# Performance work log

Measured on AMD Instinct MI355X. Metric: run time of the kernel, lower is better.

Reference implementation:

```python
import jax, jax.numpy as jnp
import numpy as np

B, T, D, H = 2, 2048, 1024, 16
HD = D // H  # head dim = 64

def build_rope(t, half, base=10000.0):
    inv = 1.0 / (base ** (jnp.arange(0, half, dtype=jnp.float32) / half))
    ang = jnp.arange(t, dtype=jnp.float32)[:, None] * inv[None, :]  # (T, half)
    return jnp.stack([jnp.cos(ang), jnp.sin(ang)], axis=-1)  # (T, half, 2)

def setup_inputs() -> dict:
    key = jax.random.key(0)
    k1, k2, k3 = jax.random.split(key, 3)
    x = jax.random.normal(k1, (B, T, D), dtype=jnp.float32)
    W_attn = jax.random.normal(k2, (D, 3 * D), dtype=jnp.float32) * (1.0 / np.sqrt(D))
    W_proj = jax.random.normal(k3, (D, D), dtype=jnp.float32) * (1.0 / np.sqrt(D))
    rope = build_rope(T, HD // 2)
    mask = jnp.tril(jnp.ones((T, T), dtype=bool))[None, None]  # (1,1,T,T) causal
    return {"x": x, "rope": rope, "W_attn": W_attn, "W_proj": W_proj, "mask": mask}

def apply_rope(xq, rope):
    # xq: (B, T, H, HD); rope: (T, HD//2, 2)
    xs = xq.astype(jnp.float32).reshape(*xq.shape[:-1], -1, 2)        # (B,T,H,HD/2,2)
    rc = rope[:xq.shape[1]].reshape(1, xq.shape[1], 1, xs.shape[3], 2)  # (1,T,1,HD/2,2)
    out = jnp.stack([
        xs[..., 0] * rc[..., 0] - xs[..., 1] * rc[..., 1],
        xs[..., 1] * rc[..., 0] + xs[..., 0] * rc[..., 1],
    ], axis=-1)
    return out.reshape(xq.shape).astype(xq.dtype)

def reference(x, rope, W_attn, W_proj, mask):
    b, t, d = x.shape
    qkv = x @ W_attn                                   # (B,T,3D)
    q, k, v = jnp.split(qkv, 3, axis=2)
    q = apply_rope(q.reshape(b, t, H, HD), rope)
    k = apply_rope(k.reshape(b, t, H, HD), rope)
    v = v.reshape(b, t, H, HD)
    # (B,H,T,HD)
    q = q.transpose(0, 2, 1, 3)
    k = k.transpose(0, 2, 1, 3)
    v = v.transpose(0, 2, 1, 3)
    scale = 1.0 / np.sqrt(HD)
    scores = jnp.einsum('bhqd,bhkd->bhqk', q, k) * scale
    scores = jnp.where(mask, scores, jnp.finfo(scores.dtype).min)
    attn = jax.nn.softmax(scores, axis=-1)
    out = jnp.einsum('bhqk,bhkd->bhqd', attn, v)       # (B,H,T,HD)
    out = out.transpose(0, 2, 1, 3).reshape(b, t, d)
    return out @ W_proj
```

## Files before the change

kernel.cpp:

```cpp
#include <hip/hip_runtime.h>


typedef __bf16 bf16x8 __attribute__((ext_vector_type(8)));
typedef float f32x4 __attribute__((ext_vector_type(4)));

__device__ __forceinline__ float bf2f(unsigned short u) {
  unsigned int i = ((unsigned int)u) << 16;
  return __builtin_bit_cast(float, i);
}
__device__ __forceinline__ unsigned short f2bf(float f) {
  unsigned int i = __builtin_bit_cast(unsigned int, f);
  i += 0x7FFFu + ((i >> 16) & 1u);
  return (unsigned short)(i >> 16);
}

__device__ __forceinline__ void gload_lds16(const unsigned short* g, unsigned short* l) {
  __builtin_amdgcn_global_load_lds(
      (const __attribute__((address_space(1))) void*)g,
      (__attribute__((address_space(3))) void*)l, 16, 0, 0);
}

__global__ __launch_bounds__(256) void convert_f32_bf16_kernel(
    const float* __restrict__ in, unsigned short* __restrict__ outp, int n8)
{
  int i = blockIdx.x * 256 + threadIdx.x;
  if (i >= n8) return;
  const float4 a0 = *reinterpret_cast<const float4*>(&in[(size_t)i * 8]);
  const float4 a1 = *reinterpret_cast<const float4*>(&in[(size_t)i * 8 + 4]);
  uint4 pk;
  pk.x = (unsigned int)f2bf(a0.x) | ((unsigned int)f2bf(a0.y) << 16);
  pk.y = (unsigned int)f2bf(a0.z) | ((unsigned int)f2bf(a0.w) << 16);
  pk.z = (unsigned int)f2bf(a1.x) | ((unsigned int)f2bf(a1.y) << 16);
  pk.w = (unsigned int)f2bf(a1.z) | ((unsigned int)f2bf(a1.w) << 16);
  *reinterpret_cast<uint4*>(&outp[(size_t)i * 8]) = pk;
}

__global__ __launch_bounds__(256) void convert_transpose_kernel(
    const float* __restrict__ W, unsigned short* __restrict__ WT, int R, int C)
{
  __shared__ unsigned short tileT[64][72];
  const int c0 = blockIdx.x * 64, r0 = blockIdx.y * 64;
  const int tid = threadIdx.x;
  const int rr = tid >> 4, cc = (tid & 15) * 4;
#pragma unroll
  for (int it = 0; it < 4; ++it) {
    int gr = r0 + rr + it * 16;
    float4 v = *reinterpret_cast<const float4*>(&W[(size_t)gr * C + c0 + cc]);
    tileT[cc + 0][rr + it * 16] = f2bf(v.x);
    tileT[cc + 1][rr + it * 16] = f2bf(v.y);
    tileT[cc + 2][rr + it * 16] = f2bf(v.z);
    tileT[cc + 3][rr + it * 16] = f2bf(v.w);
  }
  __syncthreads();
  const int wc = tid >> 2, wk = (tid & 3) * 16;
  uint4 o0 = *reinterpret_cast<const uint4*>(&tileT[wc][wk]);
  uint4 o1 = *reinterpret_cast<const uint4*>(&tileT[wc][wk + 8]);
  unsigned short* dst = &WT[(size_t)(c0 + wc) * R + r0 + wk];
  *reinterpret_cast<uint4*>(dst) = o0;
  *reinterpret_cast<uint4*>(dst + 8) = o1;
}

__global__ __launch_bounds__(256) void transpose_v_kernel(
    const unsigned short* __restrict__ Vb, unsigned short* __restrict__ VT)
{
  __shared__ unsigned short tl[64][72];
  const int bh = blockIdx.y;
  const int t0 = blockIdx.x * 64;
  const int tid = threadIdx.x;
  const unsigned short* src = Vb + (size_t)bh * 2048 * 64;
  unsigned short* dst = VT + (size_t)bh * 64 * 2048;
  int row = tid >> 3, c8 = (tid & 7) * 8;
#pragma unroll
  for (int it = 0; it < 2; ++it, row += 32) {
    uint4 v = *reinterpret_cast<const uint4*>(&src[(size_t)(t0 + row) * 64 + c8]);
    *reinterpret_cast<uint4*>(&tl[row][c8]) = v;
  }
  __syncthreads();
  const int d = tid >> 2, tc = (tid & 3) * 16;
  unsigned int o[8];
#pragma unroll
  for (int j = 0; j < 8; ++j) {
    unsigned int lo  = tl[tc + 2 * j][d];
    unsigned int hi2 = tl[tc + 2 * j + 1][d];
    o[j] = lo | (hi2 << 16);
  }
  unsigned short* dp = &dst[(size_t)d * 2048 + t0 + tc];
  *reinterpret_cast<uint4*>(dp)     = uint4{o[0], o[1], o[2], o[3]};
  *reinterpret_cast<uint4*>(dp + 8) = uint4{o[4], o[5], o[6], o[7]};
}

template<bool C_IS_F32>
__global__ __launch_bounds__(256) void gemm_bt_kernel(
    const unsigned short* __restrict__ A, const unsigned short* __restrict__ BT,
    void* __restrict__ Cp, int M, int N, int K)
{
  __shared__ alignas(16) unsigned short As[128 * 32];
  __shared__ alignas(16) unsigned short Bs[128 * 32];

  const int tid = threadIdx.x;
  const int m0 = blockIdx.y * 128, n0 = blockIdx.x * 128;
  const int w = tid >> 6, lane = tid & 63;
  const int wr = (w >> 1) * 64, wc = (w & 1) * 64;
  const int g = lane >> 4, r = lane & 15;

  f32x4 acc[4][4];
#pragma unroll
  for (int i = 0; i < 4; ++i)
#pragma unroll
    for (int j = 0; j < 4; ++j)
      acc[i][j] = f32x4{0.f, 0.f, 0.f, 0.f};

  const int srow = w * 32 + (lane >> 2);
  const int sk = (lane & 3) << 3;
  const size_t a_base = (size_t)(m0 + srow) * K + sk;
  const size_t b_base = (size_t)(n0 + srow) * K + sk;
  unsigned short* lA = &As[w * 1024 + lane * 8];
  unsigned short* lB = &Bs[w * 1024 + lane * 8];
  const size_t rstep = (size_t)16 * K;

  for (int k0 = 0; k0 < K; k0 += 32) {
    __syncthreads();
    gload_lds16(&A[a_base + k0], lA);
    gload_lds16(&A[a_base + k0 + rstep], lA + 512);
    gload_lds16(&BT[b_base + k0], lB);
    gload_lds16(&BT[b_base + k0 + rstep], lB + 512);
    __syncthreads();

    bf16x8 af[4], bff[4];
#pragma unroll
    for (int i = 0; i < 4; ++i)
      af[i] = __builtin_bit_cast(bf16x8,
          *reinterpret_cast<const uint4*>(&As[(wr + i * 16 + r) * 32 + g * 8]));
#pragma unroll
    for (int j = 0; j < 4; ++j)
      bff[j] = __builtin_bit_cast(bf16x8,
          *reinterpret_cast<const uint4*>(&Bs[(wc + j * 16 + r) * 32 + g * 8]));
#pragma unroll
    for (int i = 0; i < 4; ++i)
#pragma unroll
      for (int j = 0; j < 4; ++j)
        acc[i][j] = __builtin_amdgcn_mfma_f32_16x16x32_bf16(af[i], bff[j], acc[i][j], 0, 0, 0);
  }

#pragma unroll
  for (int i = 0; i < 4; ++i)
#pragma unroll
    for (int j = 0; j < 4; ++j)
#pragma unroll
      for (int reg = 0; reg < 4; ++reg) {
        int row = m0 + wr + i * 16 + g * 4 + reg;
        int col = n0 + wc + j * 16 + r;
        if constexpr (C_IS_F32)
          ((float*)Cp)[(size_t)row * N + col] = acc[i][j][reg];
        else
          ((unsigned short*)Cp)[(size_t)row * N + col] = f2bf(acc[i][j][reg]);
      }
}

__global__ __launch_bounds__(256) void rope_scatter_kernel(
    const unsigned short* __restrict__ qkv, const float* __restrict__ rope,
    unsigned short* __restrict__ Qb, unsigned short* __restrict__ Kb,
    unsigned short* __restrict__ Vb)
{
  int gid = blockIdx.x * 256 + threadIdx.x;
  int rowM = gid / 768;
  int c4 = (gid - rowM * 768) * 4;
  int b = rowM >> 11, t = rowM & 2047;
  int sec = c4 >> 10;
  int d = c4 & 1023;
  int h = d >> 6, hd = d & 63;

  uint2 vv = *reinterpret_cast<const uint2*>(&qkv[(size_t)rowM * 3072 + c4]);
  size_t dst = ((size_t)(b * 16 + h) * 2048 + t) * 64 + hd;

  if (sec == 2) {
    *reinterpret_cast<uint2*>(&Vb[dst]) = vv;
    return;
  }
  float x0 = bf2f((unsigned short)(vv.x & 0xffffu));
  float x1 = bf2f((unsigned short)(vv.x >> 16));
  float x2 = bf2f((unsigned short)(vv.y & 0xffffu));
  float x3 = bf2f((unsigned short)(vv.y >> 16));
  float4 rc = *reinterpret_cast<const float4*>(&rope[(size_t)t * 64 + hd]);
  float y0 = x0 * rc.x - x1 * rc.y;
  float y1 = x1 * rc.x + x0 * rc.y;
  float y2 = x2 * rc.z - x3 * rc.w;
  float y3 = x3 * rc.z + x2 * rc.w;
  uint2 outv;
  outv.x = (unsigned int)f2bf(y0) | ((unsigned int)f2bf(y1) << 16);
  outv.y = (unsigned int)f2bf(y2) | ((unsigned int)f2bf(y3) << 16);
  unsigned short* dstp = (sec == 0) ? Qb : Kb;
  *reinterpret_cast<uint2*>(&dstp[dst]) = outv;
}

__global__ __launch_bounds__(512, 4) void attn_mfma_kernel(
    const unsigned short* __restrict__ Q, const unsigned short* __restrict__ K,
    const unsigned short* __restrict__ VT, unsigned short* __restrict__ O)
{
  __shared__ unsigned short Ks[2][64 * 64];
  __shared__ unsigned short Vs[2][64 * 64];
  __shared__ unsigned short Ps[8][16 * 64];

  const int bx = blockIdx.x;
  const int idx = bx & 255, hi = bx >> 8;
  const int bh = hi * 16 + (idx >> 4);
  const int tp = idx & 15;
  const int tile = hi ? tp : 15 - tp;
  const int b = bh >> 4, h = bh & 15;
  const size_t base = (size_t)bh * 2048 * 64;
  const unsigned short* VTb = VT + (size_t)bh * 64 * 2048;

  const int tid = threadIdx.x, w = tid >> 6, lane = tid & 63;
  const int g = lane >> 4, r = lane & 15;
  const int q0 = tile * 128;
  const int wrow0 = q0 + w * 16;

  bf16x8 qf[2];
#pragma unroll
  for (int kk = 0; kk < 2; ++kk)
    qf[kk] = __builtin_bit_cast(bf16x8, *reinterpret_cast<const uint4*>(
        &Q[base + (size_t)(wrow0 + r) * 64 + kk * 32 + g * 8]));

  float m[4], l[4];
  f32x4 ov[4];
#pragma unroll
  for (int reg = 0; reg < 4; ++reg) { m[reg] = -1e30f; l[reg] = 0.f; }
#pragma unroll
  for (int df = 0; df < 4; ++df) ov[df] = f32x4{0.f, 0.f, 0.f, 0.f};

  const int srow = tid >> 3, sc8 = (tid & 7) * 8;
  const unsigned short* Kg = &K[base + (size_t)srow * 64 + sc8];
  const unsigned short* Vg = &VTb[(size_t)srow * 2048 + sc8];
  const int sb = srow * 128 + ((sc8 * 2) ^ ((srow & 7) << 4));

  unsigned short* Pw = &Ps[w][0];
  const float cs = 0.125f * 1.44269504f;
  const int nkt = (q0 >> 6) + 2;

  uint4 kreg = *reinterpret_cast<const uint4*>(Kg);
  uint4 vreg = *reinterpret_cast<const uint4*>(Vg);
  *reinterpret_cast<uint4*>((char*)Ks[0] + sb) = kreg;
  *reinterpret_cast<uint4*>((char*)Vs[0] + sb) = vreg;
  __syncthreads();

  for (int c = 0; c < nkt; ++c) {
    const int kb = c * 64;
    const int cur = c & 1;
    const bool pfn = (c + 1 < nkt);
    if (pfn) {
      kreg = *reinterpret_cast<const uint4*>(Kg + (size_t)(kb + 64) * 64);
      vreg = *reinterpret_cast<const uint4*>(Vg + kb + 64);
    }

    if (kb <= wrow0 + 15) {
      f32x4 s[4];
#pragma unroll
      for (int cf = 0; cf < 4; ++cf) s[cf] = f32x4{0.f, 0.f, 0.f, 0.f};
      __builtin_amdgcn_s_setprio(1);
#pragma unroll
      for (int kk = 0; kk < 2; ++kk) {
#pragma unroll
        for (int cf = 0; cf < 4; ++cf) {
          int row = cf * 16 + r;
          const char* p = (const char*)Ks[cur] + row * 128 + ((kk * 64 + g * 16) ^ ((r & 7) << 4));
          bf16x8 kf = __builtin_bit_cast(bf16x8, *reinterpret_cast<const uint4*>(p));
          s[cf] = __builtin_amdgcn_mfma_f32_16x16x32_bf16(qf[kk], kf, s[cf], 0, 0, 0);
        }
      }
      __builtin_amdgcn_s_setprio(0);

      if (kb + 63 > wrow0) {
#pragma unroll
        for (int cf = 0; cf < 4; ++cf) {
          int key = kb + cf * 16 + r;
#pragma unroll
          for (int reg = 0; reg < 4; ++reg) {
            int rowg = wrow0 + g * 4 + reg;
            if (key > rowg) s[cf][reg] = -1e30f;
          }
        }
      }

      f32x4 alv;
#pragma unroll
      for (int reg = 0; reg < 4; ++reg) {
        float v = fmaxf(fmaxf(s[0][reg], s[1][reg]), fmaxf(s[2][reg], s[3][reg]));
        v = fmaxf(v, __shfl_xor(v, 1));
        v = fmaxf(v, __shfl_xor(v, 2));
        v = fmaxf(v, __shfl_xor(v, 4));
        v = fmaxf(v, __shfl_xor(v, 8));
        float mo = m[reg];
        float mn = fmaxf(mo, v);
        float al = __builtin_amdgcn_exp2f((mo - mn) * cs);
        m[reg] = mn;
        float ps = 0.f;
        int rowp = g * 4 + reg;
        char* prow = (char*)Pw + rowp * 128;
        int sw = (rowp & 7) << 4;
#pragma unroll
        for (int cf = 0; cf < 4; ++cf) {
          float p = __builtin_amdgcn_exp2f((s[cf][reg] - mn) * cs);
          ps += p;
          *reinterpret_cast<unsigned short*>(prow + (((cf * 16 + r) * 2) ^ sw)) = f2bf(p);
        }
        l[reg] = l[reg] * al + ps;
        alv[reg] = al;
      }
#pragma unroll
      for (int df = 0; df < 4; ++df) ov[df] *= alv;

      __builtin_amdgcn_s_setprio(1);
#pragma unroll
      for (int kk = 0; kk < 2; ++kk) {
        const char* pp = (const char*)Pw + r * 128 + ((kk * 64 + g * 16) ^ ((r & 7) << 4));
        bf16x8 pf = __builtin_bit_cast(bf16x8, *reinterpret_cast<const uint4*>(pp));
#pragma unroll
        for (int df = 0; df < 4; ++df) {
          int row = df * 16 + r;
          const char* p = (const char*)Vs[cur] + row * 128 + ((kk * 64 + g * 16) ^ ((r & 7) << 4));
          bf16x8 vf = __builtin_bit_cast(bf16x8, *reinterpret_cast<const uint4*>(p));
          ov[df] = __builtin_amdgcn_mfma_f32_16x16x32_bf16(pf, vf, ov[df], 0, 0, 0);
        }
      }
      __builtin_amdgcn_s_setprio(0);
    }

    if (pfn) {
      *reinterpret_cast<uint4*>((char*)Ks[cur ^ 1] + sb) = kreg;
      *reinterpret_cast<uint4*>((char*)Vs[cur ^ 1] + sb) = vreg;
    }
    __syncthreads();
  }

#pragma unroll
  for (int reg = 0; reg < 4; ++reg) {
    float ls = l[reg];
    ls += __shfl_xor(ls, 1);
    ls += __shfl_xor(ls, 2);
    ls += __shfl_xor(ls, 4);
    ls += __shfl_xor(ls, 8);
    float inv = 1.f / ls;
    int rowg = wrow0 + g * 4 + reg;
    size_t ob = (size_t)(b * 2048 + rowg) * 1024 + h * 64;
#pragma unroll
    for (int df = 0; df < 4; ++df)
      O[ob + df * 16 + r] = f2bf(ov[df][reg] * inv);
  }
}

extern "C" void kernel_launch(void* const* d_in, const int* in_sizes, int n_in,
                              void* d_out, int out_size, void* d_ws, size_t ws_size,
                              hipStream_t stream)
{
  (void)in_sizes; (void)n_in; (void)out_size; (void)ws_size;
  const float* x    = (const float*)d_in[0];
  const float* rope = (const float*)d_in[1];
  const float* Wa   = (const float*)d_in[2];
  const float* Wp   = (const float*)d_in[3];

  unsigned short* ws  = (unsigned short*)d_ws;
  unsigned short* qkv = ws;
  unsigned short* Qb  = qkv + (size_t)4096 * 3072;
  unsigned short* Kb  = Qb + (size_t)32 * 2048 * 64;
  unsigned short* Vb  = Kb + (size_t)32 * 2048 * 64;
  unsigned short* WpT = Vb + (size_t)32 * 2048 * 64;
  unsigned short* xb  = Qb;
  unsigned short* WaT = Kb;
  unsigned short* O   = qkv;
  unsigned short* VT  = qkv + (size_t)4096 * 1024;
  float* out = (float*)d_out;

  convert_f32_bf16_kernel<<<2048, 256, 0, stream>>>(x, xb, 4096 * 1024 / 8);
  convert_transpose_kernel<<<dim3(48, 16), 256, 0, stream>>>(Wa, WaT, 1024, 3072);
  convert_transpose_kernel<<<dim3(16, 16), 256, 0, stream>>>(Wp, WpT, 1024, 1024);
  gemm_bt_kernel<false><<<dim3(3072 / 128, 4096 / 128), 256, 0, stream>>>(
      xb, WaT, qkv, 4096, 3072, 1024);
  rope_scatter_kernel<<<(4096 * 3072 / 4) / 256, 256, 0, stream>>>(qkv, rope, Qb, Kb, Vb);
  transpose_v_kernel<<<dim3(32, 32), 256, 0, stream>>>(Vb, VT);
  attn_mfma_kernel<<<512, 512, 0, stream>>>(Qb, Kb, VT, O);
  gemm_bt_kernel<true><<<dim3(1024 / 128, 4096 / 128), 256, 0, stream>>>(
      O, WpT, out, 4096, 1024, 1024);
}
```

Measured before the change: 233.3 us.

## Transpose attention MFMA operands to keep P in registers via lane shuffles

Swaps the MFMA operand order so that S and O are computed transposed, which puts each query row in a single lane. The per-row softmax max and sum then need only two cross-lane shuffles instead of four per register. P is passed to the PV MFMA through __shfl lane permutations instead of being written to and reread from a per-wave LDS buffer, and the output store becomes a vectorised 8-byte write. This removes the Ps LDS traffic and its shared-memory footprint. In exchange it adds 16 ds_bpermute shuffles per tile and relies on the shuffle indexing being correct.

```diff
diff --git a/kernel.cpp b/kernel.cpp
--- a/kernel.cpp
+++ b/kernel.cpp
@@ -12,6 +12,9 @@
   unsigned int i = __builtin_bit_cast(unsigned int, f);
   i += 0x7FFFu + ((i >> 16) & 1u);
   return (unsigned short)(i >> 16);
+}
+__device__ __forceinline__ unsigned int pack2(float a, float b) {
+  return (unsigned int)f2bf(a) | ((unsigned int)f2bf(b) << 16);
 }
 
 __device__ __forceinline__ void gload_lds16(const unsigned short* g, unsigned short* l) {
@@ -28,10 +31,10 @@
   const float4 a0 = *reinterpret_cast<const float4*>(&in[(size_t)i * 8]);
   const float4 a1 = *reinterpret_cast<const float4*>(&in[(size_t)i * 8 + 4]);
   uint4 pk;
-  pk.x = (unsigned int)f2bf(a0.x) | ((unsigned int)f2bf(a0.y) << 16);
-  pk.y = (unsigned int)f2bf(a0.z) | ((unsigned int)f2bf(a0.w) << 16);
-  pk.z = (unsigned int)f2bf(a1.x) | ((unsigned int)f2bf(a1.y) << 16);
-  pk.w = (unsigned int)f2bf(a1.z) | ((unsigned int)f2bf(a1.w) << 16);
+  pk.x = pack2(a0.x, a0.y);
+  pk.y = pack2(a0.z, a0.w);
+  pk.z = pack2(a1.x, a1.y);
+  pk.w = pack2(a1.z, a1.w);
   *reinterpret_cast<uint4*>(&outp[(size_t)i * 8]) = pk;
 }
 
@@ -187,8 +190,8 @@
   float y2 = x2 * rc.z - x3 * rc.w;
   float y3 = x3 * rc.z + x2 * rc.w;
   uint2 outv;
-  outv.x = (unsigned int)f2bf(y0) | ((unsigned int)f2bf(y1) << 16);
-  outv.y = (unsigned int)f2bf(y2) | ((unsigned int)f2bf(y3) << 16);
+  outv.x = pack2(y0, y1);
+  outv.y = pack2(y2, y3);
   unsigned short* dstp = (sec == 0) ? Qb : Kb;
   *reinterpret_cast<uint2*>(&dstp[dst]) = outv;
 }
@@ -199,7 +202,6 @@
 {
   __shared__ unsigned short Ks[2][64 * 64];
   __shared__ unsigned short Vs[2][64 * 64];
-  __shared__ unsigned short Ps[8][16 * 64];
 
   const int bx = blockIdx.x;
   const int idx = bx & 255, hi = bx >> 8;
@@ -221,10 +223,8 @@
     qf[kk] = __builtin_bit_cast(bf16x8, *reinterpret_cast<const uint4*>(
         &Q[base + (size_t)(wrow0 + r) * 64 + kk * 32 + g * 8]));
 
-  float m[4], l[4];
+  float m = -1e30f, l = 0.f;
   f32x4 ov[4];
-#pragma unroll
-  for (int reg = 0; reg < 4; ++reg) { m[reg] = -1e30f; l[reg] = 0.f; }
 #pragma unroll
   for (int df = 0; df < 4; ++df) ov[df] = f32x4{0.f, 0.f, 0.f, 0.f};
 
@@ -233,9 +233,12 @@
   const unsigned short* Vg = &VTb[(size_t)srow * 2048 + sc8];
   const int sb = srow * 128 + ((sc8 * 2) ^ ((srow & 7) << 4));
 
-  unsigned short* Pw = &Ps[w][0];
   const float cs = 0.125f * 1.44269504f;
   const int nkt = (q0 >> 6) + 2;
+
+  const int srcA = ((g & 1) << 5) | r;
+  const int srcB = srcA | 16;
+  const bool hsel = (g >> 1) != 0;
 
   uint4 kreg = *reinterpret_cast<const uint4*>(Kg);
   uint4 vreg = *reinterpret_cast<const uint4*>(Vg);
@@ -264,7 +267,7 @@
           int row = cf * 16 + r;
           const char* p = (const char*)Ks[cur] + row * 128 + ((kk * 64 + g * 16) ^ ((r & 7) << 4));
           bf16x8 kf = __builtin_bit_cast(bf16x8, *reinterpret_cast<const uint4*>(p));
-          s[cf] = __builtin_amdgcn_mfma_f32_16x16x32_bf16(qf[kk], kf, s[cf], 0, 0, 0);
+          s[cf] = __builtin_amdgcn_mfma_f32_16x16x32_bf16(kf, qf[kk], s[cf], 0, 0, 0);
         }
       }
       __builtin_amdgcn_s_setprio(0);
@@ -272,54 +275,60 @@
       if (kb + 63 > wrow0) {
 #pragma unroll
         for (int cf = 0; cf < 4; ++cf) {
-          int key = kb + cf * 16 + r;
-#pragma unroll
-          for (int reg = 0; reg < 4; ++reg) {
-            int rowg = wrow0 + g * 4 + reg;
-            if (key > rowg) s[cf][reg] = -1e30f;
-          }
+          int keyb = kb + cf * 16 + g * 4;
+#pragma unroll
+          for (int reg = 0; reg < 4; ++reg)
+            if (keyb + reg > wrow0 + r) s[cf][reg] = -1e30f;
         }
       }
 
-      f32x4 alv;
-#pragma unroll
-      for (int reg = 0; reg < 4; ++reg) {
-        float v = fmaxf(fmaxf(s[0][reg], s[1][reg]), fmaxf(s[2][reg], s[3][reg]));
-        v = fmaxf(v, __shfl_xor(v, 1));
-        v = fmaxf(v, __shfl_xor(v, 2));
-        v = fmaxf(v, __shfl_xor(v, 4));
-        v = fmaxf(v, __shfl_xor(v, 8));
-        float mo = m[reg];
-        float mn = fmaxf(mo, v);
-        float al = __builtin_amdgcn_exp2f((mo - mn) * cs);
-        m[reg] = mn;
-        float ps = 0.f;
-        int rowp = g * 4 + reg;
-        char* prow = (char*)Pw + rowp * 128;
-        int sw = (rowp & 7) << 4;
-#pragma unroll
-        for (int cf = 0; cf < 4; ++cf) {
+      float vmx = s[0][0];
+#pragma unroll
+      for (int cf = 0; cf < 4; ++cf)
+#pragma unroll
+        for (int reg = 0; reg < 4; ++reg)
+          vmx = fmaxf(vmx, s[cf][reg]);
+      vmx = fmaxf(vmx, __shfl_xor(vmx, 16));
+      vmx = fmaxf(vmx, __shfl_xor(vmx, 32));
+      float mo = m;
+      float mn = fmaxf(mo, vmx);
+      float al = __builtin_amdgcn_exp2f((mo - mn) * cs);
+      m = mn;
+      float ps = 0.f;
+#pragma unroll
+      for (int cf = 0; cf < 4; ++cf)
+#pragma unroll
+        for (int reg = 0; reg < 4; ++reg) {
           float p = __builtin_amdgcn_exp2f((s[cf][reg] - mn) * cs);
+          s[cf][reg] = p;
           ps += p;
-          *reinterpret_cast<unsigned short*>(prow + (((cf * 16 + r) * 2) ^ sw)) = f2bf(p);
         }
-        l[reg] = l[reg] * al + ps;
-        alv[reg] = al;
-      }
-#pragma unroll
-      for (int df = 0; df < 4; ++df) ov[df] *= alv;
+      l = l * al + ps;
+#pragma unroll
+      for (int df = 0; df < 4; ++df) ov[df] *= al;
+
+      unsigned int pk[4][2];
+#pragma unroll
+      for (int cf = 0; cf < 4; ++cf) {
+        pk[cf][0] = pack2(s[cf][0], s[cf][1]);
+        pk[cf][1] = pack2(s[cf][2], s[cf][3]);
+      }
 
       __builtin_amdgcn_s_setprio(1);
 #pragma unroll
       for (int kk = 0; kk < 2; ++kk) {
-        const char* pp = (const char*)Pw + r * 128 + ((kk * 64 + g * 16) ^ ((r & 7) << 4));
-        bf16x8 pf = __builtin_bit_cast(bf16x8, *reinterpret_cast<const uint4*>(pp));
+        unsigned int a0 = __shfl(pk[2 * kk][0], srcA), b0 = __shfl(pk[2 * kk + 1][0], srcA);
+        unsigned int a1 = __shfl(pk[2 * kk][1], srcA), b1 = __shfl(pk[2 * kk + 1][1], srcA);
+        unsigned int a2 = __shfl(pk[2 * kk][0], srcB), b2 = __shfl(pk[2 * kk + 1][0], srcB);
+        unsigned int a3 = __shfl(pk[2 * kk][1], srcB), b3 = __shfl(pk[2 * kk + 1][1], srcB);
+        uint4 pw{ hsel ? b0 : a0, hsel ? b1 : a1, hsel ? b2 : a2, hsel ? b3 : a3 };
+        bf16x8 pf = __builtin_bit_cast(bf16x8, pw);
 #pragma unroll
         for (int df = 0; df < 4; ++df) {
           int row = df * 16 + r;
           const char* p = (const char*)Vs[cur] + row * 128 + ((kk * 64 + g * 16) ^ ((r & 7) << 4));
           bf16x8 vf = __builtin_bit_cast(bf16x8, *reinterpret_cast<const uint4*>(p));
-          ov[df] = __builtin_amdgcn_mfma_f32_16x16x32_bf16(pf, vf, ov[df], 0, 0, 0);
+          ov[df] = __builtin_amdgcn_mfma_f32_16x16x32_bf16(vf, pf, ov[df], 0, 0, 0);
         }
       }
       __builtin_amdgcn_s_setprio(0);
@@ -332,19 +341,17 @@
     __syncthreads();
   }
 
-#pragma unroll
-  for (int reg = 0; reg < 4; ++reg) {
-    float ls = l[reg];
-    ls += __shfl_xor(ls, 1);
-    ls += __shfl_xor(ls, 2);
-    ls += __shfl_xor(ls, 4);
-    ls += __shfl_xor(ls, 8);
-    float inv = 1.f / ls;
-    int rowg = wrow0 + g * 4 + reg;
-    size_t ob = (size_t)(b * 2048 + rowg) * 1024 + h * 64;
-#pragma unroll
-    for (int df = 0; df < 4; ++df)
-      O[ob + df * 16 + r] = f2bf(ov[df][reg] * inv);
+  float ls = l;
+  ls += __shfl_xor(ls, 16);
+  ls += __shfl_xor(ls, 32);
+  float inv = 1.f / ls;
+  size_t orow = (size_t)(b * 2048 + wrow0 + r) * 1024 + h * 64 + g * 4;
+#pragma unroll
+  for (int df = 0; df < 4; ++df) {
+    uint2 o;
+    o.x = pack2(ov[df][0] * inv, ov[df][1] * inv);
+    o.y = pack2(ov[df][2] * inv, ov[df][3] * inv);
+    *reinterpret_cast<uint2*>(&O[orow + df * 16]) = o;
   }
 }
 
```

Measured after the change: 225.7 us. -3.2%, faster.
